# Performance work log

Measured on AMD Instinct MI355X. Metric: run time of the kernel, lower is better.

Reference implementation:

```python
import jax, jax.numpy as jnp
import numpy as np

B, N, E, DIN, H1, H2, DOUT = 2, 20000, 320000, 128, 256, 256, 128


def setup_inputs() -> dict:
    key = jax.random.key(0)
    ks = jax.random.split(key, 9)
    X = jax.random.normal(ks[0], (B, N, DIN), dtype=jnp.float32)
    edge_index = jax.random.randint(ks[1], (2, E), 0, N, dtype=jnp.int32)
    def lin(k, fan_in, fan_out):
        lim = 1.0 / np.sqrt(fan_in)
        return jax.random.uniform(k, (fan_in, fan_out), jnp.float32, -lim, lim)
    W1 = lin(ks[2], DIN, H1); b1 = jnp.zeros((H1,), jnp.float32)
    W2 = lin(ks[3], H1, H2);  b2 = jnp.zeros((H2,), jnp.float32)
    W3 = lin(ks[4], H2, DOUT); b3 = jnp.zeros((DOUT,), jnp.float32)
    prelu_a = jnp.array(0.25, jnp.float32)  # PReLU default single shared param
    return dict(X=X, W1=W1, b1=b1, W2=W2, b2=b2, W3=W3, b3=b3,
                prelu_a=prelu_a, edge_index=edge_index)


def reference(X, W1, b1, W2, b2, W3, b3, prelu_a, edge_index):
    src, dst = edge_index[0], edge_index[1]
    n = X.shape[1]
    # GCN symmetric normalization with self-loops: deg = in-degree + 1
    deg = jax.ops.segment_sum(jnp.ones_like(src, X.dtype), dst, num_segments=n) + 1.0
    dinv = jax.lax.rsqrt(deg)                      # [N]
    norm_e = dinv[src] * dinv[dst]                 # [E] edge norm
    norm_self = dinv * dinv                        # [N] self-loop norm

    def gcn(x, W, b):
        h = x @ W                                  # [N, F_out]
        agg = jax.ops.segment_sum(h[src] * norm_e[:, None], dst, num_segments=n)
        agg = agg + h * norm_self[:, None]         # add self-loop message
        return agg + b

    def prelu(x):
        return jnp.where(x >= 0, x, prelu_a * x)

    def single(x):  # x: [N, DIN]
        x = prelu(gcn(x, W1, b1))
        x = prelu(gcn(x, W2, b2))
        return gcn(x, W3, b3)

    return jax.vmap(single)(X)                     # [B, N, DOUT]
```

## Files before the change

### kernel.cpp

```cpp
#include <hip/hip_runtime.h>

#define NB 20000
#define EB 320000
#define DIN 128
#define H1D 256
#define H2D 256
#define DOUTD 128


__global__ void zero_kernel(int* __restrict__ p, int n) {
    int t = blockIdx.x * blockDim.x + threadIdx.x;
    if (t < n) p[t] = 0;
}

__global__ void hist_kernel(const int* __restrict__ dst, int* __restrict__ counts) {
    int t = blockIdx.x * blockDim.x + threadIdx.x;
    if (t < EB) atomicAdd(&counts[dst[t]], 1);
}

__global__ __launch_bounds__(1024) void scan_kernel(const int* __restrict__ counts,
                                                    int* __restrict__ row_start,
                                                    int* __restrict__ cursor,
                                                    float* __restrict__ dinv) {
    __shared__ int sums[1024];
    const int CH = (NB + 1023) / 1024;
    int t = threadIdx.x;
    int base = t * CH;
    int s = 0;
    for (int j = 0; j < CH; ++j) {
        int i = base + j;
        if (i < NB) s += counts[i];
    }
    sums[t] = s;
    __syncthreads();
    for (int off = 1; off < 1024; off <<= 1) {
        int v = (t >= off) ? sums[t - off] : 0;
        __syncthreads();
        sums[t] += v;
        __syncthreads();
    }
    int run = sums[t] - s;
    for (int j = 0; j < CH; ++j) {
        int i = base + j;
        if (i < NB) {
            row_start[i] = run;
            cursor[i] = run;
            int c = counts[i];
            run += c;
            dinv[i] = rsqrtf((float)c + 1.0f);
        }
    }
    if (t == 1023) row_start[NB] = sums[1023];
}

__global__ void scatter_kernel(const int* __restrict__ src, const int* __restrict__ dst,
                               const float* __restrict__ dinv,
                               int* __restrict__ cursor, int2* __restrict__ edges) {
    int t = blockIdx.x * blockDim.x + threadIdx.x;
    if (t < EB) {
        int d = dst[t], s = src[t];
        int p = atomicAdd(&cursor[d], 1);
        edges[p] = make_int2(s, __float_as_int(dinv[s] * dinv[d]));
    }
}


__device__ inline void vload(float (&d)[4], const float* p) {
    float4 t = *(const float4*)p; d[0] = t.x; d[1] = t.y; d[2] = t.z; d[3] = t.w;
}
__device__ inline void vload(float (&d)[2], const float* p) {
    float2 t = *(const float2*)p; d[0] = t.x; d[1] = t.y;
}
__device__ inline void vstore(float* p, const float (&d)[4]) {
    *(float4*)p = make_float4(d[0], d[1], d[2], d[3]);
}
__device__ inline void vstore(float* p, const float (&d)[2]) {
    *(float2*)p = make_float2(d[0], d[1]);
}

template <int F, bool BIAS, bool PRELU>
__global__ __launch_bounds__(256) void agg_kernel(
    const float* __restrict__ h, float* __restrict__ out,
    const int* __restrict__ row_start, const int2* __restrict__ edges,
    const float* __restrict__ dinv, const float* __restrict__ bias,
    const float* __restrict__ pa, int nnodes) {
    constexpr int VEC = F / 64;
    int wid = threadIdx.x >> 6;
    int lane = threadIdx.x & 63;
    int g = blockIdx.x * 4 + wid;
    if (g >= nnodes) return;
    int icsr = g;
    int hbase = 0;
    if (icsr >= NB) { icsr -= NB; hbase = NB; }
    const float* hsrc = h + (size_t)hbase * F + (size_t)lane * VEC;
    const float* hown = h + (size_t)g * F + (size_t)lane * VEC;

    float acc0[VEC], acc1[VEC] = {}, acc2[VEC] = {}, acc3[VEC] = {};
    float dv = dinv[icsr];
    float sw = dv * dv;
    {
        float t[VEC];
        vload(t, hown);
#pragma unroll
        for (int v = 0; v < VEC; ++v) acc0[v] = t[v] * sw;
    }
    int e0 = __builtin_amdgcn_readfirstlane(row_start[icsr]);
    int e1 = __builtin_amdgcn_readfirstlane(row_start[icsr + 1]);
    int e = e0;
    for (; e + 4 <= e1; e += 4) {
        int2 ed0 = edges[e], ed1 = edges[e + 1], ed2 = edges[e + 2], ed3 = edges[e + 3];
        float t0[VEC], t1[VEC], t2[VEC], t3[VEC];
        vload(t0, hsrc + (size_t)ed0.x * F);
        vload(t1, hsrc + (size_t)ed1.x * F);
        vload(t2, hsrc + (size_t)ed2.x * F);
        vload(t3, hsrc + (size_t)ed3.x * F);
        float w0 = __int_as_float(ed0.y), w1 = __int_as_float(ed1.y);
        float w2 = __int_as_float(ed2.y), w3 = __int_as_float(ed3.y);
#pragma unroll
        for (int v = 0; v < VEC; ++v) {
            acc0[v] = fmaf(t0[v], w0, acc0[v]);
            acc1[v] = fmaf(t1[v], w1, acc1[v]);
            acc2[v] = fmaf(t2[v], w2, acc2[v]);
            acc3[v] = fmaf(t3[v], w3, acc3[v]);
        }
    }
    for (; e < e1; ++e) {
        int2 ed = edges[e];
        float t[VEC];
        vload(t, hsrc + (size_t)ed.x * F);
        float w = __int_as_float(ed.y);
#pragma unroll
        for (int v = 0; v < VEC; ++v) acc0[v] = fmaf(t[v], w, acc0[v]);
    }
#pragma unroll
    for (int v = 0; v < VEC; ++v) acc0[v] += (acc1[v] + acc2[v]) + acc3[v];
    if (BIAS) {
        float bv[VEC];
        vload(bv, bias + lane * VEC);
#pragma unroll
        for (int v = 0; v < VEC; ++v) acc0[v] += bv[v];
    }
    if (PRELU) {
        float a = *pa;
#pragma unroll
        for (int v = 0; v < VEC; ++v) acc0[v] = acc0[v] >= 0.0f ? acc0[v] : a * acc0[v];
    }
    vstore(out + (size_t)g * F + lane * VEC, acc0);
}

template <bool BIAS, bool PRELU>
__global__ __launch_bounds__(256) void gemm_kernel(const float* __restrict__ A, int M, int K,
                                                   const float* __restrict__ W, int Nc,
                                                   const float* __restrict__ bias,
                                                   const float* __restrict__ pa,
                                                   float* __restrict__ C) {
    __shared__ alignas(16) float As[16][68];
    __shared__ alignas(16) float Bs[16][68];
    int t = threadIdx.x;
    int bm = blockIdx.x * 64;
    int bn = blockIdx.y * 64;
    int tx = t & 15, ty = t >> 4;
    int m0 = ty * 4, n0 = tx * 4;
    int ar = t >> 2, ac4 = (t & 3) * 4;
    int br = t >> 4, bc4 = (t & 15) * 4;

    float acc[4][4] = {};

    for (int k0 = 0; k0 < K; k0 += 16) {
        float4 av = make_float4(0.f, 0.f, 0.f, 0.f);
        int arow = bm + ar;
        if (arow < M) av = *(const float4*)&A[(size_t)arow * K + k0 + ac4];
        As[ac4 + 0][ar] = av.x;
        As[ac4 + 1][ar] = av.y;
        As[ac4 + 2][ar] = av.z;
        As[ac4 + 3][ar] = av.w;
        float4 bv = *(const float4*)&W[(size_t)(k0 + br) * Nc + bn + bc4];
        *(float4*)&Bs[br][bc4] = bv;
        __syncthreads();
#pragma unroll
        for (int k = 0; k < 16; ++k) {
            float4 av4 = *(const float4*)&As[k][m0];
            float4 bv4 = *(const float4*)&Bs[k][n0];
            float a_[4] = {av4.x, av4.y, av4.z, av4.w};
            float b_[4] = {bv4.x, bv4.y, bv4.z, bv4.w};
#pragma unroll
            for (int i = 0; i < 4; ++i)
#pragma unroll
                for (int j = 0; j < 4; ++j)
                    acc[i][j] = fmaf(a_[i], b_[j], acc[i][j]);
        }
        __syncthreads();
    }

    float pav = 0.0f;
    if (PRELU) pav = *pa;
#pragma unroll
    for (int i = 0; i < 4; ++i) {
        int row = bm + m0 + i;
        if (row < M) {
            float v[4];
#pragma unroll
            for (int j = 0; j < 4; ++j) {
                float x = acc[i][j];
                if (BIAS) x += bias[bn + n0 + j];
                if (PRELU) x = (x >= 0.0f) ? x : pav * x;
                v[j] = x;
            }
            *(float4*)&C[(size_t)row * Nc + bn + n0] = make_float4(v[0], v[1], v[2], v[3]);
        }
    }
}


static inline char* carve(char*& p, size_t bytes) {
    char* r = p;
    p += (bytes + 255) & ~(size_t)255;
    return r;
}

extern "C" void kernel_launch(void* const* d_in, const int* in_sizes, int n_in,
                              void* d_out, int out_size, void* d_ws, size_t ws_size,
                              hipStream_t stream) {
    const float* X  = (const float*)d_in[0];
    const float* W1 = (const float*)d_in[1];
    const float* b1 = (const float*)d_in[2];
    const float* W2 = (const float*)d_in[3];
    const float* b2 = (const float*)d_in[4];
    const float* W3 = (const float*)d_in[5];
    const float* b3 = (const float*)d_in[6];
    const float* pa = (const float*)d_in[7];
    const int* ei   = (const int*)d_in[8];
    const int* src = ei;
    const int* dst = ei + EB;
    float* out = (float*)d_out;

    char* p = (char*)d_ws;
    int* counts    = (int*)carve(p, NB * sizeof(int));
    int* row_start = (int*)carve(p, (NB + 1) * sizeof(int));
    int* cursor    = (int*)carve(p, NB * sizeof(int));
    int2* edges    = (int2*)carve(p, EB * sizeof(int2));
    float* dinv    = (float*)carve(p, NB * sizeof(float));

    size_t fixed = (size_t)(p - (char*)d_ws);
    size_t need_fused = fixed + 2 * ((size_t)2 * NB * 256 * sizeof(float) + 256);
    bool fused = ws_size >= need_fused;
    size_t rows = fused ? 2 * NB : NB;
    float* bufA = (float*)carve(p, rows * 256 * sizeof(float));
    float* bufB = (float*)carve(p, rows * 256 * sizeof(float));

    zero_kernel<<<(NB + 255) / 256, 256, 0, stream>>>(counts, NB);
    hist_kernel<<<(EB + 255) / 256, 256, 0, stream>>>(dst, counts);
    scan_kernel<<<1, 1024, 0, stream>>>(counts, row_start, cursor, dinv);
    scatter_kernel<<<(EB + 255) / 256, 256, 0, stream>>>(src, dst, dinv, cursor, edges);

    int nbatch_loops = fused ? 1 : 2;
    for (int b = 0; b < nbatch_loops; ++b) {
        const float* Xb = X + (size_t)b * NB * DIN;
        float* outb = out + (size_t)b * NB * DOUTD;
        int M = (int)rows;
        int aggGrid = (M + 3) / 4;

        agg_kernel<128, false, false><<<aggGrid, 256, 0, stream>>>(
            Xb, bufA, row_start, edges, dinv, nullptr, nullptr, M);
        gemm_kernel<true, true><<<dim3((M + 63) / 64, H1D / 64), 256, 0, stream>>>(
            bufA, M, DIN, W1, H1D, b1, pa, bufB);

        gemm_kernel<false, false><<<dim3((M + 63) / 64, H2D / 64), 256, 0, stream>>>(
            bufB, M, H1D, W2, H2D, nullptr, nullptr, bufA);
        agg_kernel<256, true, true><<<aggGrid, 256, 0, stream>>>(
            bufA, bufB, row_start, edges, dinv, b2, pa, M);

        gemm_kernel<false, false><<<dim3((M + 63) / 64, DOUTD / 64), 256, 0, stream>>>(
            bufB, M, H2D, W3, DOUTD, nullptr, nullptr, bufA);
        agg_kernel<128, true, false><<<aggGrid, 256, 0, stream>>>(
            bufA, outb, row_start, edges, dinv, b3, nullptr, M);
    }
}
```

Measured before the change: 414.7 us.

## Bin CSR edges by source tile and aggregate eight rows per wave

The CSR build now keys edges by (dst, src>>12), splitting each destination's neighbours into five source-tile bins, with a separate dinv kernel. The aggregation kernel has each wave handle eight destination rows and walk all rows tile by tile, so gathers from the same source range land close in time and should reuse L2. This costs five times more bins, a larger single-block scan, more rs lookups and fewer waves. Per-wave ILP falls to two interleaved rows instead of four independent accumulators.

```diff
diff --git a/kernel.cpp b/kernel.cpp
--- a/kernel.cpp
+++ b/kernel.cpp
@@ -7,29 +7,37 @@
 #define H2D 256
 #define DOUTD 128
 
+#define TILE_SHIFT 12
+#define NT 5
+#define NBINS (NB * NT)
+#define RPW 8
+
 
 __global__ void zero_kernel(int* __restrict__ p, int n) {
     int t = blockIdx.x * blockDim.x + threadIdx.x;
     if (t < n) p[t] = 0;
 }
 
-__global__ void hist_kernel(const int* __restrict__ dst, int* __restrict__ counts) {
+__global__ void hist_kernel(const int* __restrict__ src, const int* __restrict__ dst,
+                            int* __restrict__ bins) {
     int t = blockIdx.x * blockDim.x + threadIdx.x;
-    if (t < EB) atomicAdd(&counts[dst[t]], 1);
-}
-
-__global__ __launch_bounds__(1024) void scan_kernel(const int* __restrict__ counts,
-                                                    int* __restrict__ row_start,
-                                                    int* __restrict__ cursor,
-                                                    float* __restrict__ dinv) {
+    if (t < EB) {
+        int key = dst[t] * NT + (src[t] >> TILE_SHIFT);
+        atomicAdd(&bins[key], 1);
+    }
+}
+
+__global__ __launch_bounds__(1024) void scan_kernel(const int* __restrict__ bins,
+                                                    int* __restrict__ rs,
+                                                    int* __restrict__ cursor) {
     __shared__ int sums[1024];
-    const int CH = (NB + 1023) / 1024;
+    const int CH = (NBINS + 1023) / 1024;
     int t = threadIdx.x;
     int base = t * CH;
     int s = 0;
     for (int j = 0; j < CH; ++j) {
         int i = base + j;
-        if (i < NB) s += counts[i];
+        if (i < NBINS) s += bins[i];
     }
     sums[t] = s;
     __syncthreads();
@@ -42,15 +50,21 @@
     int run = sums[t] - s;
     for (int j = 0; j < CH; ++j) {
         int i = base + j;
-        if (i < NB) {
-            row_start[i] = run;
+        if (i < NBINS) {
+            rs[i] = run;
             cursor[i] = run;
-            int c = counts[i];
-            run += c;
-            dinv[i] = rsqrtf((float)c + 1.0f);
-        }
-    }
-    if (t == 1023) row_start[NB] = sums[1023];
+            run += bins[i];
+        }
+    }
+    if (t == 1023) rs[NBINS] = sums[1023];
+}
+
+__global__ void dinv_kernel(const int* __restrict__ rs, float* __restrict__ dinv) {
+    int i = blockIdx.x * blockDim.x + threadIdx.x;
+    if (i < NB) {
+        int deg = rs[(i + 1) * NT] - rs[i * NT];
+        dinv[i] = rsqrtf((float)deg + 1.0f);
+    }
 }
 
 __global__ void scatter_kernel(const int* __restrict__ src, const int* __restrict__ dst,
@@ -59,7 +73,8 @@
     int t = blockIdx.x * blockDim.x + threadIdx.x;
     if (t < EB) {
         int d = dst[t], s = src[t];
-        int p = atomicAdd(&cursor[d], 1);
+        int key = d * NT + (s >> TILE_SHIFT);
+        int p = atomicAdd(&cursor[key], 1);
         edges[p] = make_int2(s, __float_as_int(dinv[s] * dinv[d]));
     }
 }
@@ -78,74 +93,93 @@
     *(float2*)p = make_float2(d[0], d[1]);
 }
 
+template <int F, int VEC>
+__device__ inline void drain(const float* __restrict__ hsrc, const int2* __restrict__ edges,
+                             int e0, int e1, float (&acc)[VEC]) {
+    int e = e0;
+    for (; e + 2 <= e1; e += 2) {
+        int2 r0 = edges[e], r1 = edges[e + 1];
+        float t0[VEC], t1[VEC];
+        vload(t0, hsrc + (size_t)r0.x * F);
+        vload(t1, hsrc + (size_t)r1.x * F);
+        float w0 = __int_as_float(r0.y), w1 = __int_as_float(r1.y);
+#pragma unroll
+        for (int v = 0; v < VEC; ++v) acc[v] = fmaf(t0[v], w0, acc[v]);
+#pragma unroll
+        for (int v = 0; v < VEC; ++v) acc[v] = fmaf(t1[v], w1, acc[v]);
+    }
+    if (e < e1) {
+        int2 r0 = edges[e];
+        float t0[VEC];
+        vload(t0, hsrc + (size_t)r0.x * F);
+        float w0 = __int_as_float(r0.y);
+#pragma unroll
+        for (int v = 0; v < VEC; ++v) acc[v] = fmaf(t0[v], w0, acc[v]);
+    }
+}
+
 template <int F, bool BIAS, bool PRELU>
-__global__ __launch_bounds__(256) void agg_kernel(
+__global__ __launch_bounds__(256) void agg2_kernel(
     const float* __restrict__ h, float* __restrict__ out,
-    const int* __restrict__ row_start, const int2* __restrict__ edges,
+    const int* __restrict__ rs, const int2* __restrict__ edges,
     const float* __restrict__ dinv, const float* __restrict__ bias,
-    const float* __restrict__ pa, int nnodes) {
+    const float* __restrict__ pa, int nrows) {
     constexpr int VEC = F / 64;
-    int wid = threadIdx.x >> 6;
+    int w = blockIdx.x * 4 + (threadIdx.x >> 6);
     int lane = threadIdx.x & 63;
-    int g = blockIdx.x * 4 + wid;
-    if (g >= nnodes) return;
-    int icsr = g;
-    int hbase = 0;
-    if (icsr >= NB) { icsr -= NB; hbase = NB; }
-    const float* hsrc = h + (size_t)hbase * F + (size_t)lane * VEC;
-    const float* hown = h + (size_t)g * F + (size_t)lane * VEC;
-
-    float acc0[VEC], acc1[VEC] = {}, acc2[VEC] = {}, acc3[VEC] = {};
-    float dv = dinv[icsr];
-    float sw = dv * dv;
-    {
+    int base = w * RPW;
+    if (base >= nrows) return;
+    int hb = (base >= NB) ? NB : 0;
+    int ic = base - hb;
+    const float* hsrc = h + (size_t)hb * F + lane * VEC;
+
+    float acc[RPW][VEC];
+#pragma unroll
+    for (int r = 0; r < RPW; ++r) {
+        float dv = dinv[ic + r];
         float t[VEC];
-        vload(t, hown);
-#pragma unroll
-        for (int v = 0; v < VEC; ++v) acc0[v] = t[v] * sw;
-    }
-    int e0 = __builtin_amdgcn_readfirstlane(row_start[icsr]);
-    int e1 = __builtin_amdgcn_readfirstlane(row_start[icsr + 1]);
-    int e = e0;
-    for (; e + 4 <= e1; e += 4) {
-        int2 ed0 = edges[e], ed1 = edges[e + 1], ed2 = edges[e + 2], ed3 = edges[e + 3];
-        float t0[VEC], t1[VEC], t2[VEC], t3[VEC];
-        vload(t0, hsrc + (size_t)ed0.x * F);
-        vload(t1, hsrc + (size_t)ed1.x * F);
-        vload(t2, hsrc + (size_t)ed2.x * F);
-        vload(t3, hsrc + (size_t)ed3.x * F);
-        float w0 = __int_as_float(ed0.y), w1 = __int_as_float(ed1.y);
-        float w2 = __int_as_float(ed2.y), w3 = __int_as_float(ed3.y);
+        vload(t, h + (size_t)(base + r) * F + lane * VEC);
+#pragma unroll
+        for (int v = 0; v < VEC; ++v) acc[r][v] = t[v] * (dv * dv);
+    }
+
+    for (int tt = 0; tt < NT; ++tt) {
+#pragma unroll
+        for (int r = 0; r < RPW; r += 2) {
+            int ka = (ic + r) * NT + tt;
+            int kb = ka + NT;
+            int a0 = rs[ka], a1 = rs[ka + 1];
+            int b0 = rs[kb], b1 = rs[kb + 1];
+            while (a0 < a1 && b0 < b1) {
+                int2 ra = edges[a0++], rb = edges[b0++];
+                float ta[VEC], tb[VEC];
+                vload(ta, hsrc + (size_t)ra.x * F);
+                vload(tb, hsrc + (size_t)rb.x * F);
+                float wa = __int_as_float(ra.y), wb = __int_as_float(rb.y);
+#pragma unroll
+                for (int v = 0; v < VEC; ++v) acc[r][v] = fmaf(ta[v], wa, acc[r][v]);
+#pragma unroll
+                for (int v = 0; v < VEC; ++v) acc[r + 1][v] = fmaf(tb[v], wb, acc[r + 1][v]);
+            }
+            drain<F, VEC>(hsrc, edges, a0, a1, acc[r]);
+            drain<F, VEC>(hsrc, edges, b0, b1, acc[r + 1]);
+        }
+    }
+
+    float bv[VEC];
+    if (BIAS) vload(bv, bias + lane * VEC);
+    float a = PRELU ? *pa : 0.0f;
+#pragma unroll
+    for (int r = 0; r < RPW; ++r) {
 #pragma unroll
         for (int v = 0; v < VEC; ++v) {
-            acc0[v] = fmaf(t0[v], w0, acc0[v]);
-            acc1[v] = fmaf(t1[v], w1, acc1[v]);
-            acc2[v] = fmaf(t2[v], w2, acc2[v]);
-            acc3[v] = fmaf(t3[v], w3, acc3[v]);
-        }
-    }
-    for (; e < e1; ++e) {
-        int2 ed = edges[e];
-        float t[VEC];
-        vload(t, hsrc + (size_t)ed.x * F);
-        float w = __int_as_float(ed.y);
-#pragma unroll
-        for (int v = 0; v < VEC; ++v) acc0[v] = fmaf(t[v], w, acc0[v]);
-    }
-#pragma unroll
-    for (int v = 0; v < VEC; ++v) acc0[v] += (acc1[v] + acc2[v]) + acc3[v];
-    if (BIAS) {
-        float bv[VEC];
-        vload(bv, bias + lane * VEC);
-#pragma unroll
-        for (int v = 0; v < VEC; ++v) acc0[v] += bv[v];
-    }
-    if (PRELU) {
-        float a = *pa;
-#pragma unroll
-        for (int v = 0; v < VEC; ++v) acc0[v] = acc0[v] >= 0.0f ? acc0[v] : a * acc0[v];
-    }
-    vstore(out + (size_t)g * F + lane * VEC, acc0);
+            float x = acc[r][v];
+            if (BIAS) x += bv[v];
+            if (PRELU) x = (x >= 0.0f) ? x : a * x;
+            acc[r][v] = x;
+        }
+        vstore(out + (size_t)(base + r) * F + lane * VEC, acc[r]);
+    }
 }
 
 template <bool BIAS, bool PRELU>
@@ -235,11 +269,11 @@
     float* out = (float*)d_out;
 
     char* p = (char*)d_ws;
-    int* counts    = (int*)carve(p, NB * sizeof(int));
-    int* row_start = (int*)carve(p, (NB + 1) * sizeof(int));
-    int* cursor    = (int*)carve(p, NB * sizeof(int));
-    int2* edges    = (int2*)carve(p, EB * sizeof(int2));
-    float* dinv    = (float*)carve(p, NB * sizeof(float));
+    int* bins   = (int*)carve(p, NBINS * sizeof(int));
+    int* rs     = (int*)carve(p, (NBINS + 1) * sizeof(int));
+    int* cursor = (int*)carve(p, NBINS * sizeof(int));
+    int2* edges = (int2*)carve(p, EB * sizeof(int2));
+    float* dinv = (float*)carve(p, NB * sizeof(float));
 
     size_t fixed = (size_t)(p - (char*)d_ws);
     size_t need_fused = fixed + 2 * ((size_t)2 * NB * 256 * sizeof(float) + 256);
@@ -248,9 +282,10 @@
     float* bufA = (float*)carve(p, rows * 256 * sizeof(float));
     float* bufB = (float*)carve(p, rows * 256 * sizeof(float));
 
-    zero_kernel<<<(NB + 255) / 256, 256, 0, stream>>>(counts, NB);
-    hist_kernel<<<(EB + 255) / 256, 256, 0, stream>>>(dst, counts);
-    scan_kernel<<<1, 1024, 0, stream>>>(counts, row_start, cursor, dinv);
+    zero_kernel<<<(NBINS + 255) / 256, 256, 0, stream>>>(bins, NBINS);
+    hist_kernel<<<(EB + 255) / 256, 256, 0, stream>>>(src, dst, bins);
+    scan_kernel<<<1, 1024, 0, stream>>>(bins, rs, cursor);
+    dinv_kernel<<<(NB + 255) / 256, 256, 0, stream>>>(rs, dinv);
     scatter_kernel<<<(EB + 255) / 256, 256, 0, stream>>>(src, dst, dinv, cursor, edges);
 
     int nbatch_loops = fused ? 1 : 2;
@@ -258,21 +293,21 @@
         const float* Xb = X + (size_t)b * NB * DIN;
         float* outb = out + (size_t)b * NB * DOUTD;
         int M = (int)rows;
-        int aggGrid = (M + 3) / 4;
-
-        agg_kernel<128, false, false><<<aggGrid, 256, 0, stream>>>(
-            Xb, bufA, row_start, edges, dinv, nullptr, nullptr, M);
+        int aggGrid = (M + 4 * RPW - 1) / (4 * RPW);
+
+        agg2_kernel<128, false, false><<<aggGrid, 256, 0, stream>>>(
+            Xb, bufA, rs, edges, dinv, nullptr, nullptr, M);
         gemm_kernel<true, true><<<dim3((M + 63) / 64, H1D / 64), 256, 0, stream>>>(
             bufA, M, DIN, W1, H1D, b1, pa, bufB);
 
         gemm_kernel<false, false><<<dim3((M + 63) / 64, H2D / 64), 256, 0, stream>>>(
             bufB, M, H1D, W2, H2D, nullptr, nullptr, bufA);
-        agg_kernel<256, true, true><<<aggGrid, 256, 0, stream>>>(
-            bufA, bufB, row_start, edges, dinv, b2, pa, M);
+        agg2_kernel<256, true, true><<<aggGrid, 256, 0, stream>>>(
+            bufA, bufB, rs, edges, dinv, b2, pa, M);
 
         gemm_kernel<false, false><<<dim3((M + 63) / 64, DOUTD / 64), 256, 0, stream>>>(
             bufB, M, H2D, W3, DOUTD, nullptr, nullptr, bufA);
-        agg_kernel<128, true, false><<<aggGrid, 256, 0, stream>>>(
-            bufA, outb, row_start, edges, dinv, b3, nullptr, M);
-    }
-}
+        agg2_kernel<128, true, false><<<aggGrid, 256, 0, stream>>>(
+            bufA, outb, rs, edges, dinv, b3, nullptr, M);
+    }
+}
```

Measured after the change: 675.2 us. 1.63x slower.
